# Kernel optimization log

Measured on AMD Instinct MI355X. Metric: run time of the kernel, lower is better.

The kernel has to match this reference:

```python
import jax, jax.numpy as jnp
import numpy as np

N = 50000
E = 625000
D_IN = 128
D_OUT = 128
NEG_SLOPE = 0.01  # torch LeakyReLU default


def setup_inputs() -> dict:
    key = jax.random.key(0)
    k1, k2, k3, k4, k5, k6, k7, k8 = jax.random.split(key, 8)
    features = jax.random.normal(k1, (N, D_IN), dtype=jnp.float32)
    target = jax.random.randint(k2, (E,), 0, N, dtype=jnp.int64)
    neighbor = jax.random.randint(k3, (E,), 0, N, dtype=jnp.int64)
    values = jax.random.uniform(k4, (E,), dtype=jnp.float32)
    # nn.Linear params (kaiming-uniform-ish init: U(-1/sqrt(in), 1/sqrt(in)))
    bound = 1.0 / np.sqrt(D_IN)
    W1 = jax.random.uniform(k5, (D_OUT, D_IN), minval=-bound, maxval=bound, dtype=jnp.float32)
    b1 = jax.random.uniform(k6, (D_OUT,), minval=-bound, maxval=bound, dtype=jnp.float32)
    W2 = jax.random.uniform(k7, (D_OUT, D_IN), minval=-bound, maxval=bound, dtype=jnp.float32)
    b2 = jax.random.uniform(k8, (D_OUT,), minval=-bound, maxval=bound, dtype=jnp.float32)
    return {"features": features, "target": target, "neighbor": neighbor,
            "values": values, "W1": W1, "b1": b1, "W2": W2, "b2": b2}


def reference(features, target, neighbor, values, W1, b1, W2, b2):
    # gather-scale: msg[e] = features[neighbor[e]] * values[e]
    msg = features[neighbor] * values[:, None]              # (E, D_IN)
    # scatter-add into target nodes
    h_neigh = jax.ops.segment_sum(msg, target, num_segments=N)  # (N, D_IN)
    # dual linear fusion + leaky relu
    h = (features + h_neigh) @ W1.T + b1 + (features * h_neigh) @ W2.T + b2
    return jnp.where(h >= 0, h, NEG_SLOPE * h)
```

## Files before the change

kernel.cpp:

```cpp
#include <hip/hip_runtime.h>

#define D 128
#define CAP 32
#define EPT 8
#define NEG_SLOPE 0.01f

typedef float v4f __attribute__((ext_vector_type(4)));
typedef short short8 __attribute__((ext_vector_type(8)));

static __device__ __forceinline__ short f2bf(float f) {
    unsigned u = __float_as_uint(f);
    unsigned r = (u + 0x7fffu + ((u >> 16) & 1u)) >> 16;
    return (short)r;
}
static __device__ __forceinline__ float bflo(unsigned u) { return __uint_as_float(u << 16); }
static __device__ __forceinline__ float bfhi(unsigned u) { return __uint_as_float(u & 0xffff0000u); }
static __device__ __forceinline__ unsigned packbf(float x, float y) {
    return (unsigned)(unsigned short)f2bf(x) | ((unsigned)(unsigned short)f2bf(y) << 16);
}

__global__ __launch_bounds__(256) void convbucket_kernel(const float* __restrict__ feat,
                                                         const float* __restrict__ W1,
                                                         const float* __restrict__ W2,
                                                         const int* __restrict__ tgt,
                                                         const int* __restrict__ nbr,
                                                         const float* __restrict__ vals,
                                                         unsigned* __restrict__ featbf,
                                                         short* __restrict__ Wbf,
                                                         int* __restrict__ deg,
                                                         unsigned* __restrict__ edata,
                                                         int4* __restrict__ ovf,
                                                         int* __restrict__ ovf_cnt,
                                                         int nQuads, int E, int nbB) {
    if ((int)blockIdx.x < nbB) {
        int base = (blockIdx.x * 256 + threadIdx.x) * EPT;
#pragma unroll
        for (int k = 0; k < EPT; k++) {
            int e = base + k;
            if (e < E) {
                int t    = tgt[e];
                int slot = atomicAdd(&deg[t], 1);
                if (slot < CAP) {
                    unsigned ent = ((unsigned)nbr[e] << 16) |
                                   (unsigned)(unsigned short)f2bf(vals[e]);
                    edata[((unsigned)t << 5) + slot] = ent;
                } else {
                    int o = atomicAdd(ovf_cnt, 1);
                    int4 ov;
                    ov.x = t;
                    ov.y = nbr[e];
                    ov.z = __float_as_int(vals[e]);
                    ov.w = 0;
                    ovf[o] = ov;
                }
            }
        }
    } else {
        int i = (blockIdx.x - nbB) * 256 + threadIdx.x;
        if (i < nQuads) {
            float4 f = ((const float4*)feat)[i];
            uint2 p;
            p.x = packbf(f.x, f.y);
            p.y = packbf(f.z, f.w);
            ((uint2*)featbf)[i] = p;
        }
        if (i < D * D) {
            Wbf[i]         = f2bf(W1[i]);
            Wbf[D * D + i] = f2bf(W2[i]);
        }
    }
}

__global__ __launch_bounds__(256) void gathergemm_kernel(const unsigned* __restrict__ featbf,
                                                         const unsigned* __restrict__ edata,
                                                         const int* __restrict__ deg,
                                                         const int4* __restrict__ ovf,
                                                         const int* __restrict__ ovf_cnt,
                                                         const short* __restrict__ Wbf,
                                                         const float* __restrict__ b1,
                                                         const float* __restrict__ b2,
                                                         float* __restrict__ out,
                                                         int nNodes) {
    __shared__ __align__(16) unsigned sX[4][2][1024];

    int tid  = threadIdx.x;
    int lane = tid & 63;
    int w    = tid >> 6;
    int tile = blockIdx.x * 4 + w;
    int m0   = tile * 16;
    if (m0 >= nNodes) return;

    int mrow = lane & 15;
    int quad = lane >> 4;

    float bias[8];
#pragma unroll
    for (int ot = 0; ot < 8; ot++) {
        int o = ot * 16 + mrow;
        bias[ot] = b1[o] + b2[o];
    }

    int degv = deg[min(m0 + mrow, nNodes - 1)];

    for (int n = 0; n < 16; n++) {
        int node = m0 + n;
        int d    = (node < nNodes) ? __shfl(degv, n) : 0;
        int dd   = d < CAP ? d : CAP;

        unsigned uf = featbf[(long)min(node, nNodes - 1) * (D / 2) + lane];

        float ax0 = 0.f, ay0 = 0.f, ax1 = 0.f, ay1 = 0.f;
        float ax2 = 0.f, ay2 = 0.f, ax3 = 0.f, ay3 = 0.f;

        {
            const unsigned* ep = edata + ((unsigned)node << 5);
            int dm1 = dd - 1;
            for (int j = 0; j < dd; j += 8) {
                unsigned p0 = ep[min(j + 0, dm1)];
                unsigned p1 = ep[min(j + 1, dm1)];
                unsigned p2 = ep[min(j + 2, dm1)];
                unsigned p3 = ep[min(j + 3, dm1)];
                unsigned p4 = ep[min(j + 4, dm1)];
                unsigned p5 = ep[min(j + 5, dm1)];
                unsigned p6 = ep[min(j + 6, dm1)];
                unsigned p7 = ep[min(j + 7, dm1)];
                unsigned u0 = featbf[(long)(p0 >> 16) * (D / 2) + lane];
                unsigned u1 = featbf[(long)(p1 >> 16) * (D / 2) + lane];
                unsigned u2 = featbf[(long)(p2 >> 16) * (D / 2) + lane];
                unsigned u3 = featbf[(long)(p3 >> 16) * (D / 2) + lane];
                unsigned u4 = featbf[(long)(p4 >> 16) * (D / 2) + lane];
                unsigned u5 = featbf[(long)(p5 >> 16) * (D / 2) + lane];
                unsigned u6 = featbf[(long)(p6 >> 16) * (D / 2) + lane];
                unsigned u7 = featbf[(long)(p7 >> 16) * (D / 2) + lane];
                float v0 = (j + 0 < dd) ? bflo(p0) : 0.0f;
                float v1 = (j + 1 < dd) ? bflo(p1) : 0.0f;
                float v2 = (j + 2 < dd) ? bflo(p2) : 0.0f;
                float v3 = (j + 3 < dd) ? bflo(p3) : 0.0f;
                float v4 = (j + 4 < dd) ? bflo(p4) : 0.0f;
                float v5 = (j + 5 < dd) ? bflo(p5) : 0.0f;
                float v6 = (j + 6 < dd) ? bflo(p6) : 0.0f;
                float v7 = (j + 7 < dd) ? bflo(p7) : 0.0f;
                ax0 += bflo(u0) * v0; ay0 += bfhi(u0) * v0;
                ax1 += bflo(u1) * v1; ay1 += bfhi(u1) * v1;
                ax2 += bflo(u2) * v2; ay2 += bfhi(u2) * v2;
                ax3 += bflo(u3) * v3; ay3 += bfhi(u3) * v3;
                ax0 += bflo(u4) * v4; ay0 += bfhi(u4) * v4;
                ax1 += bflo(u5) * v5; ay1 += bfhi(u5) * v5;
                ax2 += bflo(u6) * v6; ay2 += bfhi(u6) * v6;
                ax3 += bflo(u7) * v7; ay3 += bfhi(u7) * v7;
            }
        }

        if (d > CAP) {
            int cnt = *ovf_cnt;
            for (int basek = 0; basek < cnt; basek += 64) {
                int k = basek + lane;
                int t = (k < cnt) ? ovf[k].x : -1;
                unsigned long long m = __ballot(t == node);
                while (m) {
                    int b = __ffsll((long long)m) - 1;
                    m &= m - 1;
                    int4  ov = ovf[basek + b];
                    float v  = __int_as_float(ov.z);
                    unsigned u = featbf[(long)ov.y * (D / 2) + lane];
                    ax0 += bflo(u) * v;
                    ay0 += bfhi(u) * v;
                }
            }
        }

        float accx = (ax0 + ax1) + (ax2 + ax3);
        float accy = (ay0 + ay1) + (ay2 + ay3);
        float fx = bflo(uf), fy = bfhi(uf);
        int idx = n * 64 + (((lane >> 2) ^ n) << 2) + (lane & 3);
        sX[w][0][idx] = packbf(fx + accx, fy + accy);
        sX[w][1][idx] = packbf(fx * accx, fy * accy);
    }

    v4f acc[8];
#pragma unroll
    for (int ot = 0; ot < 8; ot++) acc[ot] = (v4f)(0.0f);

#pragma unroll
    for (int s = 0; s < 4; s++) {
        int ck = s * 4 + quad;
        int pp = ck ^ mrow;
        short8 a1 = *(const short8*)(&sX[w][0][mrow * 64 + pp * 4]);
        short8 a2 = *(const short8*)(&sX[w][1][mrow * 64 + pp * 4]);
        const short* wp = Wbf + ck * 8;
#pragma unroll
        for (int ot = 0; ot < 8; ot++) {
            int row = ot * 16 + mrow;
            short8 w1 = *(const short8*)(wp + row * D);
            short8 w2 = *(const short8*)(wp + D * D + row * D);
            acc[ot] = __builtin_amdgcn_mfma_f32_16x16x32_bf16(a1, w1, acc[ot], 0, 0, 0);
            acc[ot] = __builtin_amdgcn_mfma_f32_16x16x32_bf16(a2, w2, acc[ot], 0, 0, 0);
        }
    }

#pragma unroll
    for (int ot = 0; ot < 8; ot++) {
        int o = ot * 16 + mrow;
#pragma unroll
        for (int r = 0; r < 4; r++) {
            int node = m0 + quad * 4 + r;
            if (node < nNodes) {
                float v = acc[ot][r] + bias[ot];
                out[(long)node * D + o] = (v >= 0.0f) ? v : NEG_SLOPE * v;
            }
        }
    }
}

extern "C" void kernel_launch(void* const* d_in, const int* in_sizes, int n_in,
                              void* d_out, int out_size, void* d_ws, size_t ws_size,
                              hipStream_t stream) {
    const float* feat = (const float*)d_in[0];
    const int*   tgt  = (const int*)d_in[1];
    const int*   nbr  = (const int*)d_in[2];
    const float* vals = (const float*)d_in[3];
    const float* W1   = (const float*)d_in[4];
    const float* b1   = (const float*)d_in[5];
    const float* W2   = (const float*)d_in[6];
    const float* b2   = (const float*)d_in[7];
    float*       out  = (float*)d_out;

    int E      = in_sizes[1];
    int nNodes = out_size / D;

    int*      deg     = (int*)d_ws;
    int*      ovf_cnt = deg + nNodes;
    int4*     ovf     = (int4*)(deg + nNodes + 4);
    unsigned* edata   = (unsigned*)(ovf + E);
    short*    Wbf     = (short*)(edata + (long)nNodes * CAP);
    unsigned* featbf  = (unsigned*)(Wbf + 2 * D * D);

    int nQuads = nNodes * (D / 4);
    int nbB    = (E + 256 * EPT - 1) / (256 * EPT);
    int nbC    = (nQuads + 255) / 256;

    hipMemsetAsync(deg, 0, (size_t)(nNodes + 4) * sizeof(int), stream);
    convbucket_kernel<<<nbB + nbC, 256, 0, stream>>>(feat, W1, W2, tgt, nbr, vals,
                                                     featbf, Wbf, deg, edata, ovf, ovf_cnt,
                                                     nQuads, E, nbB);

    int nTiles  = (nNodes + 15) / 16;
    int nBlocks = (nTiles + 3) / 4;
    gathergemm_kernel<<<nBlocks, 256, 0, stream>>>(featbf, edata, deg, ovf, ovf_cnt,
                                                   Wbf, b1, b2, out, nNodes);
}
```

Baseline: 191.2 us.

## Split each 16-node tile across four waves for gather and GEMM

```diff
diff --git a/kernel.cpp b/kernel.cpp
--- a/kernel.cpp
+++ b/kernel.cpp
@@ -81,30 +81,21 @@
                                                          const float* __restrict__ b2,
                                                          float* __restrict__ out,
                                                          int nNodes) {
-    __shared__ __align__(16) unsigned sX[4][2][1024];
+    __shared__ __align__(16) unsigned sX[2][1024];
 
     int tid  = threadIdx.x;
     int lane = tid & 63;
     int w    = tid >> 6;
-    int tile = blockIdx.x * 4 + w;
-    int m0   = tile * 16;
+    int m0   = blockIdx.x * 16;
     if (m0 >= nNodes) return;
 
     int mrow = lane & 15;
     int quad = lane >> 4;
 
-    float bias[8];
-#pragma unroll
-    for (int ot = 0; ot < 8; ot++) {
-        int o = ot * 16 + mrow;
-        bias[ot] = b1[o] + b2[o];
-    }
-
-    int degv = deg[min(m0 + mrow, nNodes - 1)];
-
-    for (int n = 0; n < 16; n++) {
+    for (int k = 0; k < 4; k++) {
+        int n    = w * 4 + k;
         int node = m0 + n;
-        int d    = (node < nNodes) ? __shfl(degv, n) : 0;
+        int d    = (node < nNodes) ? deg[node] : 0;
         int dd   = d < CAP ? d : CAP;
 
         unsigned uf = featbf[(long)min(node, nNodes - 1) * (D / 2) + lane];
@@ -154,8 +145,8 @@
         if (d > CAP) {
             int cnt = *ovf_cnt;
             for (int basek = 0; basek < cnt; basek += 64) {
-                int k = basek + lane;
-                int t = (k < cnt) ? ovf[k].x : -1;
+                int kk = basek + lane;
+                int t  = (kk < cnt) ? ovf[kk].x : -1;
                 unsigned long long m = __ballot(t == node);
                 while (m) {
                     int b = __ffsll((long long)m) - 1;
@@ -173,39 +164,49 @@
         float accy = (ay0 + ay1) + (ay2 + ay3);
         float fx = bflo(uf), fy = bfhi(uf);
         int idx = n * 64 + (((lane >> 2) ^ n) << 2) + (lane & 3);
-        sX[w][0][idx] = packbf(fx + accx, fy + accy);
-        sX[w][1][idx] = packbf(fx * accx, fy * accy);
-    }
-
-    v4f acc[8];
-#pragma unroll
-    for (int ot = 0; ot < 8; ot++) acc[ot] = (v4f)(0.0f);
+        sX[0][idx] = packbf(fx + accx, fy + accy);
+        sX[1][idx] = packbf(fx * accx, fy * accy);
+    }
+
+    __syncthreads();
+
+    int ot0 = w * 2;
+    float bias[2];
+#pragma unroll
+    for (int j = 0; j < 2; j++) {
+        int o = (ot0 + j) * 16 + mrow;
+        bias[j] = b1[o] + b2[o];
+    }
+
+    v4f acc[2];
+#pragma unroll
+    for (int j = 0; j < 2; j++) acc[j] = (v4f)(0.0f);
 
 #pragma unroll
     for (int s = 0; s < 4; s++) {
         int ck = s * 4 + quad;
         int pp = ck ^ mrow;
-        short8 a1 = *(const short8*)(&sX[w][0][mrow * 64 + pp * 4]);
-        short8 a2 = *(const short8*)(&sX[w][1][mrow * 64 + pp * 4]);
+        short8 a1 = *(const short8*)(&sX[0][mrow * 64 + pp * 4]);
+        short8 a2 = *(const short8*)(&sX[1][mrow * 64 + pp * 4]);
         const short* wp = Wbf + ck * 8;
 #pragma unroll
-        for (int ot = 0; ot < 8; ot++) {
-            int row = ot * 16 + mrow;
+        for (int j = 0; j < 2; j++) {
+            int row = (ot0 + j) * 16 + mrow;
             short8 w1 = *(const short8*)(wp + row * D);
             short8 w2 = *(const short8*)(wp + D * D + row * D);
-            acc[ot] = __builtin_amdgcn_mfma_f32_16x16x32_bf16(a1, w1, acc[ot], 0, 0, 0);
-            acc[ot] = __builtin_amdgcn_mfma_f32_16x16x32_bf16(a2, w2, acc[ot], 0, 0, 0);
-        }
-    }
-
-#pragma unroll
-    for (int ot = 0; ot < 8; ot++) {
-        int o = ot * 16 + mrow;
+            acc[j] = __builtin_amdgcn_mfma_f32_16x16x32_bf16(a1, w1, acc[j], 0, 0, 0);
+            acc[j] = __builtin_amdgcn_mfma_f32_16x16x32_bf16(a2, w2, acc[j], 0, 0, 0);
+        }
+    }
+
+#pragma unroll
+    for (int j = 0; j < 2; j++) {
+        int o = (ot0 + j) * 16 + mrow;
 #pragma unroll
         for (int r = 0; r < 4; r++) {
             int node = m0 + quad * 4 + r;
             if (node < nNodes) {
-                float v = acc[ot][r] + bias[ot];
+                float v = acc[j][r] + bias[j];
                 out[(long)node * D + o] = (v >= 0.0f) ? v : NEG_SLOPE * v;
             }
         }
@@ -244,8 +245,7 @@
                                                      featbf, Wbf, deg, edata, ovf, ovf_cnt,
                                                      nQuads, E, nbB);
 
-    int nTiles  = (nNodes + 15) / 16;
-    int nBlocks = (nTiles + 3) / 4;
-    gathergemm_kernel<<<nBlocks, 256, 0, stream>>>(featbf, edata, deg, ovf, ovf_cnt,
-                                                   Wbf, b1, b2, out, nNodes);
-}
+    int nTiles = (nNodes + 15) / 16;
+    gathergemm_kernel<<<nTiles, 256, 0, stream>>>(featbf, edata, deg, ovf, ovf_cnt,
+                                                  Wbf, b1, b2, out, nNodes);
+}
```

New measurement: 181.8 us. -4.9%, faster.
